# Kernel tuning notes

Hardware: AMD Instinct MI355X
Metric: run time of the kernel (lower is better)

The kernel has to match this reference:

```python
import jax, jax.numpy as jnp
import numpy as np

B, HW, A, N, C = 32, 1600, 5, 128, 80
WIN, HIN = 1280.0, 1280.0
WOUT, HOUT = 40, 40
STRIDE = 32.0
IOU_THRESH = 0.6
OBJECT_SCALE = 5.0
NOOBJECT_SCALE = 1.0
COORD_SCALE = 1.0
CLASS_SCALE = 1.0
ANCHORS = np.array([[1.3221, 1.73145], [3.19275, 4.00944], [5.05587, 8.09892],
                    [9.47112, 4.84053], [11.2364, 10.0071]], dtype=np.float32)


def setup_inputs():
    key = jax.random.key(0)
    k1, k2, k3, k4, k5, k6, k7 = jax.random.split(key, 7)
    bbox_pred = jax.random.uniform(k1, (B, HW, A, 4), jnp.float32)   # sigmoid/exp-decoded preds in [0,1)
    iou_pred = jax.random.uniform(k2, (B, HW, A, 1), jnp.float32)
    x1 = jax.random.uniform(k3, (B, N), jnp.float32) * 1100.0
    y1 = jax.random.uniform(k4, (B, N), jnp.float32) * 1100.0
    wh = jax.random.uniform(k5, (B, N, 2), jnp.float32) * 170.0 + 8.0
    cls = jax.random.randint(k6, (B, N), 0, C).astype(jnp.float32)
    gt_boxes = jnp.stack([x1, y1, x1 + wh[..., 0], y1 + wh[..., 1], cls], axis=-1)  # (B,N,5) in-bounds
    num_boxes = jax.random.randint(k7, (B,), 1, N + 1)
    return {'bbox_pred': bbox_pred, 'iou_pred': iou_pred, 'gt_boxes': gt_boxes,
            'anchors': jnp.asarray(ANCHORS), 'num_boxes': num_boxes, 'size_index': 0}


def _forward(bbox_pred, iou_pred, gt_boxes, anchors, num_boxes, size_index):
    dt = bbox_pred.dtype
    # ---- yolo_to_bbox: decode to absolute (x1,y1,x2,y2) in input pixels ----
    ind = jnp.arange(HW)
    col = (ind % WOUT).astype(dt)[None, :, None]
    row = (ind // WOUT).astype(dt)[None, :, None]
    cxp = (bbox_pred[..., 0] + col) / WOUT
    cyp = (bbox_pred[..., 1] + row) / HOUT
    bw = bbox_pred[..., 2] * anchors[None, None, :, 0] / WOUT * 0.5
    bh = bbox_pred[..., 3] * anchors[None, None, :, 1] / HOUT * 0.5
    scale = jnp.array([WIN, HIN, WIN, HIN], dt)
    real = jnp.stack([cxp - bw, cyp - bh, cxp + bw, cyp + bh], axis=-1) * scale  # (B,HW,A,4)

    # ---- bbox_overlaps_batch: IoU of every decoded box vs every gt ----
    boxes = real.reshape(B, HW * A, 4)
    g = gt_boxes[..., :4]
    barea = (boxes[..., 2] - boxes[..., 0] + 1) * (boxes[..., 3] - boxes[..., 1] + 1)  # (B,K)
    garea = (g[..., 2] - g[..., 0] + 1) * (g[..., 3] - g[..., 1] + 1)                  # (B,N)
    iw = jnp.maximum(jnp.minimum(boxes[:, :, None, 2], g[:, None, :, 2])
                     - jnp.maximum(boxes[:, :, None, 0], g[:, None, :, 0]) + 1, 0.0)
    ih = jnp.maximum(jnp.minimum(boxes[:, :, None, 3], g[:, None, :, 3])
                     - jnp.maximum(boxes[:, :, None, 1], g[:, None, :, 1]) + 1, 0.0)
    inter = iw * ih
    ious = inter / (barea[:, :, None] + garea[:, None, :] - inter)  # (B, HW*A, N)
    ious_r = ious.reshape(B, HW, A, N)
    best = jnp.max(ious, axis=2).reshape(B, HW, A, 1)

    # no-object penalty everywhere best IoU below threshold
    iou_mask = jnp.where(best < IOU_THRESH, NOOBJECT_SCALE * (-iou_pred), jnp.zeros_like(iou_pred))

    # ---- gt -> (cell, anchor) assignment ----
    cx = (gt_boxes[..., 0] + gt_boxes[..., 2]) * 0.5 / STRIDE
    cy = (gt_boxes[..., 1] + gt_boxes[..., 3]) * 0.5 / STRIDE
    cell = (jnp.floor(cy) * WOUT + jnp.floor(cx)).astype(jnp.int32)  # (B,N)
    tw = (gt_boxes[..., 2] - gt_boxes[..., 0] + 1) / STRIDE
    th = (gt_boxes[..., 3] - gt_boxes[..., 1] + 1) / STRIDE
    # anchor_intersections: IoU of co-centered anchors vs stride-normalized gt wh
    gr = g / STRIDE
    gw = gr[..., 2] - gr[..., 0] + 1
    gh = gr[..., 3] - gr[..., 1] + 1
    aw, ah = anchors[:, 0], anchors[:, 1]
    iwa = jnp.minimum(aw[None, :, None], gw[:, None, :])
    iha = jnp.minimum(ah[None, :, None], gh[:, None, :])
    inta = iwa * iha
    a_iou = inta / ((aw * ah)[None, :, None] + (gw * gh)[:, None, :] - inta)  # (B,A,N)
    a_ind = jnp.argmax(a_iou, axis=1)  # (B,N)
    anc = anchors[a_ind]               # (B,N,2)
    tboxes = jnp.stack([cx - jnp.floor(cx), cy - jnp.floor(cy),
                        tw / anc[..., 0], th / anc[..., 1]], axis=-1)  # (B,N,4)

    # ---- vectorized scatter (replaces the python double loop) ----
    valid = (jnp.arange(N)[None, :] < num_boxes[:, None]) & (cell >= 0) & (cell < HW)
    b_idx = jnp.arange(B)[:, None]
    flat = (b_idx * HW + cell) * A + a_ind              # (B,N) index into B*HW*A
    idx = jnp.where(valid, flat, B * HW * A)            # OOB sentinel -> dropped by scatter
    safe = jnp.where(valid, flat, 0)                    # in-bounds index for gathers
    i_idx = jnp.broadcast_to(jnp.arange(N)[None, :], (B, N))

    iou_pred_f = iou_pred.reshape(-1)
    iou_mask = iou_mask.reshape(-1).at[idx].set(
        OBJECT_SCALE * (1.0 - iou_pred_f[safe]), mode='drop').reshape(B, HW, A, 1)
    ious_t = jnp.zeros(B * HW * A, dt).at[idx].set(
        ious_r.reshape(-1)[safe * N + i_idx], mode='drop').reshape(B, HW, A, 1)
    box_mask = jnp.full((B * HW * A,), 0.01, dt).at[idx].set(
        COORD_SCALE, mode='drop').reshape(B, HW, A, 1)
    boxes_t = jnp.broadcast_to(jnp.array([0.5, 0.5, 1.0, 1.0], dt), (B * HW * A, 4)).at[idx].set(
        tboxes, mode='drop').reshape(B, HW, A, 4)
    class_mask = jnp.zeros(B * HW * A, dt).at[idx].set(
        CLASS_SCALE, mode='drop').reshape(B, HW, A, 1)
    cls = gt_boxes[..., 4].astype(jnp.int32)
    idx_c = jnp.where(valid, flat * C + cls, B * HW * A * C)
    classes = jnp.zeros(B * HW * A * C, dt).at[idx_c].set(1.0, mode='drop').reshape(B, HW, A, C)

    return boxes_t, ious_t, classes, box_mask, iou_mask, class_mask


def reference(bbox_pred, iou_pred, gt_boxes, anchors, num_boxes, size_index):
    return _forward(bbox_pred, iou_pred, gt_boxes, anchors, num_boxes, size_index)
```

## Files before the change

### kernel.cpp

```cpp
#include <hip/hip_runtime.h>

#define BB     32
#define HW_    1600
#define AA     5
#define NN     128
#define CC     80
#define WOUT_  40
#define PRED_PER_B (HW_ * AA)

#define OFF_BOXES   0
#define SZ_BOXES    (BB * HW_ * AA * 4)
#define OFF_IOUS    (OFF_BOXES + SZ_BOXES)
#define SZ_IOUS     (BB * HW_ * AA)
#define OFF_CLASSES (OFF_IOUS + SZ_IOUS)
#define SZ_CLASSES  (BB * HW_ * AA * CC)
#define OFF_BMASK   (OFF_CLASSES + SZ_CLASSES)
#define SZ_BMASK    (BB * HW_ * AA)
#define OFF_IMASK   (OFF_BMASK + SZ_BMASK)
#define SZ_IMASK    (BB * HW_ * AA)
#define OFF_CMASK   (OFF_IMASK + SZ_IMASK)
#define SZ_CMASK    (BB * HW_ * AA)

__global__ __launch_bounds__(320) void yolo_passA(
    const float* __restrict__ bbox_pred, const float* __restrict__ iou_pred,
    const float* __restrict__ gt, const float* __restrict__ anchors,
    float* __restrict__ boxes_t, float* __restrict__ ious_t,
    float* __restrict__ classes, float* __restrict__ box_mask,
    float* __restrict__ iou_mask, float* __restrict__ class_mask)
{
    __shared__ float s_g[NN][5];

    const int b     = blockIdx.x / 25;
    const int chunk = blockIdx.x % 25;
    const int tid   = threadIdx.x;

    {
        float4* cbase = reinterpret_cast<float4*>(
            classes + (size_t)(b * PRED_PER_B + chunk * 320) * CC);
        float4 z; z.x = 0.f; z.y = 0.f; z.z = 0.f; z.w = 0.f;
        #pragma unroll
        for (int j = 0; j < 20; ++j)
            cbase[j * 320 + tid] = z;
    }

    for (int n = tid; n < NN; n += 320) {
        const float* gp = gt + (size_t)(b * NN + n) * 5;
        float x1 = gp[0], y1 = gp[1], x2 = gp[2], y2 = gp[3];
        s_g[n][0] = x1; s_g[n][1] = y1; s_g[n][2] = x2; s_g[n][3] = y2;
        float ga = (x2 - x1 + 1.0f) * (y2 - y1 + 1.0f);
        s_g[n][4] = 0.375f * ga;
    }
    __syncthreads();

    const int i  = chunk * 320 + tid;
    const int hw = i / AA;
    const int a  = i - hw * AA;
    const int gid = b * PRED_PER_B + i;

    const float4 p = *reinterpret_cast<const float4*>(bbox_pred + (size_t)gid * 4);
    const float col = (float)(hw % WOUT_);
    const float row = (float)(hw / WOUT_);
    const float aw = anchors[a * 2 + 0];
    const float ah = anchors[a * 2 + 1];

    const float cxp = (p.x + col) / 40.0f;
    const float cyp = (p.y + row) / 40.0f;
    const float bw  = p.z * aw / 40.0f * 0.5f;
    const float bh  = p.w * ah / 40.0f * 0.5f;
    const float px1 = (cxp - bw) * 1280.0f;
    const float py1 = (cyp - bh) * 1280.0f;
    const float px2 = (cxp + bw) * 1280.0f;
    const float py2 = (cyp + bh) * 1280.0f;
    const float barea = (px2 - px1 + 1.0f) * (py2 - py1 + 1.0f);
    const float thrB  = 0.375f * barea;

    bool found = false;
    #pragma unroll 4
    for (int n = 0; n < NN; ++n) {
        float iw = fminf(px2, s_g[n][2]) - fmaxf(px1, s_g[n][0]) + 1.0f;
        iw = fmaxf(iw, 0.0f);
        float ih = fminf(py2, s_g[n][3]) - fmaxf(py1, s_g[n][1]) + 1.0f;
        ih = fmaxf(ih, 0.0f);
        float inter = iw * ih;
        found |= (inter >= thrB + s_g[n][4]);
    }

    iou_mask[gid]   = found ? 0.0f : -iou_pred[gid];
    ious_t[gid]     = 0.0f;
    box_mask[gid]   = 0.01f;
    class_mask[gid] = 0.0f;
    float4 bt; bt.x = 0.5f; bt.y = 0.5f; bt.z = 1.0f; bt.w = 1.0f;
    *reinterpret_cast<float4*>(boxes_t + (size_t)gid * 4) = bt;
}

__global__ __launch_bounds__(128) void yolo_passB(
    const float* __restrict__ bbox_pred, const float* __restrict__ iou_pred,
    const float* __restrict__ gt, const float* __restrict__ anchors,
    const int* __restrict__ num_boxes,
    float* __restrict__ boxes_t, float* __restrict__ ious_t,
    float* __restrict__ classes, float* __restrict__ box_mask,
    float* __restrict__ iou_mask, float* __restrict__ class_mask)
{
    const int b = blockIdx.x;
    const int n = threadIdx.x;

    __shared__ int s_key[NN];

    const float* gp = gt + (size_t)(b * NN + n) * 5;
    const float x1 = gp[0], y1 = gp[1], x2 = gp[2], y2 = gp[3], fc = gp[4];

    const float cx  = (x1 + x2) * 0.5f / 32.0f;
    const float cy  = (y1 + y2) * 0.5f / 32.0f;
    const float fcx = floorf(cx), fcy = floorf(cy);
    const int cell  = (int)(fcy * 40.0f + fcx);
    const float tw  = (x2 - x1 + 1.0f) / 32.0f;
    const float th  = (y2 - y1 + 1.0f) / 32.0f;

    const float gx1 = x1 / 32.0f, gy1 = y1 / 32.0f;
    const float gx2 = x2 / 32.0f, gy2 = y2 / 32.0f;
    const float gw = gx2 - gx1 + 1.0f;
    const float gh = gy2 - gy1 + 1.0f;
    const float gwh = gw * gh;

    int a_ind = 0; float bestA = -1.0f;
    for (int a = 0; a < AA; ++a) {
        float aw = anchors[a * 2 + 0], ah = anchors[a * 2 + 1];
        float iwa = fminf(aw, gw), iha = fminf(ah, gh);
        float inta = iwa * iha;
        float aiou = inta / (aw * ah + gwh - inta);
        if (aiou > bestA) { bestA = aiou; a_ind = a; }
    }
    const float aw = anchors[a_ind * 2 + 0];
    const float ah = anchors[a_ind * 2 + 1];

    const bool valid = (n < num_boxes[b]) && (cell >= 0) && (cell < HW_);
    const int flat = (b * HW_ + cell) * AA + a_ind;

    s_key[n] = valid ? flat : -1;
    __syncthreads();

    if (!valid) return;

    iou_mask[flat]   = 5.0f * (1.0f - iou_pred[flat]);
    box_mask[flat]   = 1.0f;
    class_mask[flat] = 1.0f;
    classes[(size_t)flat * CC + (int)fc] = 1.0f;

    bool winner = true;
    for (int m = n + 1; m < NN; ++m)
        if (s_key[m] == flat) { winner = false; break; }
    if (!winner) return;

    const float* pp = bbox_pred + (size_t)flat * 4;
    const float col = (float)(cell % WOUT_);
    const float rw  = (float)(cell / WOUT_);
    const float cxp = (pp[0] + col) / 40.0f;
    const float cyp = (pp[1] + rw) / 40.0f;
    const float bw  = pp[2] * aw / 40.0f * 0.5f;
    const float bh  = pp[3] * ah / 40.0f * 0.5f;
    const float px1 = (cxp - bw) * 1280.0f;
    const float py1 = (cyp - bh) * 1280.0f;
    const float px2 = (cxp + bw) * 1280.0f;
    const float py2 = (cyp + bh) * 1280.0f;
    const float barea = (px2 - px1 + 1.0f) * (py2 - py1 + 1.0f);
    const float garea = (x2 - x1 + 1.0f) * (y2 - y1 + 1.0f);
    float iw = fmaxf(fminf(px2, x2) - fmaxf(px1, x1) + 1.0f, 0.0f);
    float ih = fmaxf(fminf(py2, y2) - fmaxf(py1, y1) + 1.0f, 0.0f);
    float inter = iw * ih;
    ious_t[flat] = inter / (barea + garea - inter);

    boxes_t[(size_t)flat * 4 + 0] = cx - fcx;
    boxes_t[(size_t)flat * 4 + 1] = cy - fcy;
    boxes_t[(size_t)flat * 4 + 2] = tw / aw;
    boxes_t[(size_t)flat * 4 + 3] = th / ah;
}

extern "C" void kernel_launch(void* const* d_in, const int* in_sizes, int n_in,
                              void* d_out, int out_size, void* d_ws, size_t ws_size,
                              hipStream_t stream) {
    const float* bbox_pred = (const float*)d_in[0];
    const float* iou_pred  = (const float*)d_in[1];
    const float* gt_boxes  = (const float*)d_in[2];
    const float* anchors   = (const float*)d_in[3];
    const int*   num_boxes = (const int*)d_in[4];

    float* out       = (float*)d_out;
    float* boxes_t   = out + OFF_BOXES;
    float* ious_t    = out + OFF_IOUS;
    float* classes   = out + OFF_CLASSES;
    float* box_mask  = out + OFF_BMASK;
    float* iou_mask  = out + OFF_IMASK;
    float* class_mask= out + OFF_CMASK;

    yolo_passA<<<BB * 25, 320, 0, stream>>>(
        bbox_pred, iou_pred, gt_boxes, anchors,
        boxes_t, ious_t, classes, box_mask, iou_mask, class_mask);

    yolo_passB<<<BB, NN, 0, stream>>>(
        bbox_pred, iou_pred, gt_boxes, anchors, num_boxes,
        boxes_t, ious_t, classes, box_mask, iou_mask, class_mask);
}
```

Measured before the change: 136.5 us.

## Fuse gt-assignment pass into prediction pass, removing second kernel launch

Each block now computes anchor matching and target boxes for all ground truths in shared memory. Each prediction thread scans these keys to decide whether it is the assigned cell and writes every output in a single pass. This removes the second launch and its serialization behind the first kernel. In exchange, each block redundantly computes the per-gt assignment and every thread performs an extra 128-entry key scan.

```diff
diff --git a/kernel.cpp b/kernel.cpp
--- a/kernel.cpp
+++ b/kernel.cpp
@@ -15,20 +15,21 @@
 #define OFF_CLASSES (OFF_IOUS + SZ_IOUS)
 #define SZ_CLASSES  (BB * HW_ * AA * CC)
 #define OFF_BMASK   (OFF_CLASSES + SZ_CLASSES)
-#define SZ_BMASK    (BB * HW_ * AA)
-#define OFF_IMASK   (OFF_BMASK + SZ_BMASK)
-#define SZ_IMASK    (BB * HW_ * AA)
-#define OFF_CMASK   (OFF_IMASK + SZ_IMASK)
-#define SZ_CMASK    (BB * HW_ * AA)
+#define OFF_IMASK   (OFF_BMASK + SZ_IOUS)
+#define OFF_CMASK   (OFF_IMASK + SZ_IOUS)
 
-__global__ __launch_bounds__(320) void yolo_passA(
+__global__ __launch_bounds__(320) void yolo_fused(
     const float* __restrict__ bbox_pred, const float* __restrict__ iou_pred,
     const float* __restrict__ gt, const float* __restrict__ anchors,
+    const int* __restrict__ num_boxes,
     float* __restrict__ boxes_t, float* __restrict__ ious_t,
     float* __restrict__ classes, float* __restrict__ box_mask,
     float* __restrict__ iou_mask, float* __restrict__ class_mask)
 {
     __shared__ float s_g[NN][5];
+    __shared__ int   s_key[NN];
+    __shared__ int   s_cls[NN];
+    __shared__ float s_tb[NN][4];
 
     const int b     = blockIdx.x / 25;
     const int chunk = blockIdx.x % 25;
@@ -43,21 +44,52 @@
             cbase[j * 320 + tid] = z;
     }
 
-    for (int n = tid; n < NN; n += 320) {
-        const float* gp = gt + (size_t)(b * NN + n) * 5;
+    if (tid < NN) {
+        const float* gp = gt + (size_t)(b * NN + tid) * 5;
         float x1 = gp[0], y1 = gp[1], x2 = gp[2], y2 = gp[3];
-        s_g[n][0] = x1; s_g[n][1] = y1; s_g[n][2] = x2; s_g[n][3] = y2;
-        float ga = (x2 - x1 + 1.0f) * (y2 - y1 + 1.0f);
-        s_g[n][4] = 0.375f * ga;
+        s_g[tid][0] = x1; s_g[tid][1] = y1; s_g[tid][2] = x2; s_g[tid][3] = y2;
+        s_g[tid][4] = 0.375f * ((x2 - x1 + 1.0f) * (y2 - y1 + 1.0f));
+
+        const float fc = gp[4];
+        const float cx  = (x1 + x2) * 0.5f / 32.0f;
+        const float cy  = (y1 + y2) * 0.5f / 32.0f;
+        const float fcx = floorf(cx), fcy = floorf(cy);
+        const int cell  = (int)(fcy * 40.0f + fcx);
+        const float tw  = (x2 - x1 + 1.0f) / 32.0f;
+        const float th  = (y2 - y1 + 1.0f) / 32.0f;
+
+        const float gw = (x2 / 32.0f) - (x1 / 32.0f) + 1.0f;
+        const float gh = (y2 / 32.0f) - (y1 / 32.0f) + 1.0f;
+        const float gwh = gw * gh;
+
+        int a_ind = 0; float bestA = -1.0f;
+        for (int a = 0; a < AA; ++a) {
+            float aw = anchors[a * 2 + 0], ah = anchors[a * 2 + 1];
+            float iwa = fminf(aw, gw), iha = fminf(ah, gh);
+            float inta = iwa * iha;
+            float aiou = inta / (aw * ah + gwh - inta);
+            if (aiou > bestA) { bestA = aiou; a_ind = a; }
+        }
+        const float aw = anchors[a_ind * 2 + 0];
+        const float ah = anchors[a_ind * 2 + 1];
+
+        const bool valid = (tid < num_boxes[b]) && (cell >= 0) && (cell < HW_);
+        s_key[tid]   = valid ? (cell * AA + a_ind) : -1;
+        s_cls[tid]   = (int)fc;
+        s_tb[tid][0] = cx - fcx;
+        s_tb[tid][1] = cy - fcy;
+        s_tb[tid][2] = tw / aw;
+        s_tb[tid][3] = th / ah;
     }
     __syncthreads();
 
-    const int i  = chunk * 320 + tid;
-    const int hw = i / AA;
-    const int a  = i - hw * AA;
+    const int i   = chunk * 320 + tid;
+    const int hw  = i / AA;
+    const int a   = i - hw * AA;
     const int gid = b * PRED_PER_B + i;
 
-    const float4 p = *reinterpret_cast<const float4*>(bbox_pred + (size_t)gid * 4);
+    const float4 p   = *reinterpret_cast<const float4*>(bbox_pred + (size_t)gid * 4);
+    const float ioup = iou_pred[gid];
     const float col = (float)(hw % WOUT_);
     const float row = (float)(hw / WOUT_);
     const float aw = anchors[a * 2 + 0];
@@ -81,98 +113,39 @@
         iw = fmaxf(iw, 0.0f);
         float ih = fminf(py2, s_g[n][3]) - fmaxf(py1, s_g[n][1]) + 1.0f;
         ih = fmaxf(ih, 0.0f);
-        float inter = iw * ih;
-        found |= (inter >= thrB + s_g[n][4]);
+        found |= (iw * ih >= thrB + s_g[n][4]);
     }
 
-    iou_mask[gid]   = found ? 0.0f : -iou_pred[gid];
-    ious_t[gid]     = 0.0f;
-    box_mask[gid]   = 0.01f;
-    class_mask[gid] = 0.0f;
-    float4 bt; bt.x = 0.5f; bt.y = 0.5f; bt.z = 1.0f; bt.w = 1.0f;
+    int win = -1;
+    for (int m = 0; m < NN; ++m) {
+        if (s_key[m] == i) {
+            classes[(size_t)gid * CC + s_cls[m]] = 1.0f;
+            win = m;
+        }
+    }
+    const bool sc = (win >= 0);
+
+    float iou_w = 0.0f;
+    float4 bt;
+    if (sc) {
+        const float x1 = s_g[win][0], y1 = s_g[win][1];
+        const float x2 = s_g[win][2], y2 = s_g[win][3];
+        const float garea = (x2 - x1 + 1.0f) * (y2 - y1 + 1.0f);
+        float iw = fmaxf(fminf(px2, x2) - fmaxf(px1, x1) + 1.0f, 0.0f);
+        float ih = fmaxf(fminf(py2, y2) - fmaxf(py1, y1) + 1.0f, 0.0f);
+        float inter = iw * ih;
+        iou_w = inter / (barea + garea - inter);
+        bt.x = s_tb[win][0]; bt.y = s_tb[win][1];
+        bt.z = s_tb[win][2]; bt.w = s_tb[win][3];
+    } else {
+        bt.x = 0.5f; bt.y = 0.5f; bt.z = 1.0f; bt.w = 1.0f;
+    }
+
+    iou_mask[gid]   = sc ? 5.0f * (1.0f - ioup) : (found ? 0.0f : -ioup);
+    ious_t[gid]     = iou_w;
+    box_mask[gid]   = sc ? 1.0f : 0.01f;
+    class_mask[gid] = sc ? 1.0f : 0.0f;
     *reinterpret_cast<float4*>(boxes_t + (size_t)gid * 4) = bt;
-}
-
-__global__ __launch_bounds__(128) void yolo_passB(
-    const float* __restrict__ bbox_pred, const float* __restrict__ iou_pred,
-    const float* __restrict__ gt, const float* __restrict__ anchors,
-    const int* __restrict__ num_boxes,
-    float* __restrict__ boxes_t, float* __restrict__ ious_t,
-    float* __restrict__ classes, float* __restrict__ box_mask,
-    float* __restrict__ iou_mask, float* __restrict__ class_mask)
-{
-    const int b = blockIdx.x;
-    const int n = threadIdx.x;
-
-    __shared__ int s_key[NN];
-
-    const float* gp = gt + (size_t)(b * NN + n) * 5;
-    const float x1 = gp[0], y1 = gp[1], x2 = gp[2], y2 = gp[3], fc = gp[4];
-
-    const float cx  = (x1 + x2) * 0.5f / 32.0f;
-    const float cy  = (y1 + y2) * 0.5f / 32.0f;
-    const float fcx = floorf(cx), fcy = floorf(cy);
-    const int cell  = (int)(fcy * 40.0f + fcx);
-    const float tw  = (x2 - x1 + 1.0f) / 32.0f;
-    const float th  = (y2 - y1 + 1.0f) / 32.0f;
-
-    const float gx1 = x1 / 32.0f, gy1 = y1 / 32.0f;
-    const float gx2 = x2 / 32.0f, gy2 = y2 / 32.0f;
-    const float gw = gx2 - gx1 + 1.0f;
-    const float gh = gy2 - gy1 + 1.0f;
-    const float gwh = gw * gh;
-
-    int a_ind = 0; float bestA = -1.0f;
-    for (int a = 0; a < AA; ++a) {
-        float aw = anchors[a * 2 + 0], ah = anchors[a * 2 + 1];
-        float iwa = fminf(aw, gw), iha = fminf(ah, gh);
-        float inta = iwa * iha;
-        float aiou = inta / (aw * ah + gwh - inta);
-        if (aiou > bestA) { bestA = aiou; a_ind = a; }
-    }
-    const float aw = anchors[a_ind * 2 + 0];
-    const float ah = anchors[a_ind * 2 + 1];
-
-    const bool valid = (n < num_boxes[b]) && (cell >= 0) && (cell < HW_);
-    const int flat = (b * HW_ + cell) * AA + a_ind;
-
-    s_key[n] = valid ? flat : -1;
-    __syncthreads();
-
-    if (!valid) return;
-
-    iou_mask[flat]   = 5.0f * (1.0f - iou_pred[flat]);
-    box_mask[flat]   = 1.0f;
-    class_mask[flat] = 1.0f;
-    classes[(size_t)flat * CC + (int)fc] = 1.0f;
-
-    bool winner = true;
-    for (int m = n + 1; m < NN; ++m)
-        if (s_key[m] == flat) { winner = false; break; }
-    if (!winner) return;
-
-    const float* pp = bbox_pred + (size_t)flat * 4;
-    const float col = (float)(cell % WOUT_);
-    const float rw  = (float)(cell / WOUT_);
-    const float cxp = (pp[0] + col) / 40.0f;
-    const float cyp = (pp[1] + rw) / 40.0f;
-    const float bw  = pp[2] * aw / 40.0f * 0.5f;
-    const float bh  = pp[3] * ah / 40.0f * 0.5f;
-    const float px1 = (cxp - bw) * 1280.0f;
-    const float py1 = (cyp - bh) * 1280.0f;
-    const float px2 = (cxp + bw) * 1280.0f;
-    const float py2 = (cyp + bh) * 1280.0f;
-    const float barea = (px2 - px1 + 1.0f) * (py2 - py1 + 1.0f);
-    const float garea = (x2 - x1 + 1.0f) * (y2 - y1 + 1.0f);
-    float iw = fmaxf(fminf(px2, x2) - fmaxf(px1, x1) + 1.0f, 0.0f);
-    float ih = fmaxf(fminf(py2, y2) - fmaxf(py1, y1) + 1.0f, 0.0f);
-    float inter = iw * ih;
-    ious_t[flat] = inter / (barea + garea - inter);
-
-    boxes_t[(size_t)flat * 4 + 0] = cx - fcx;
-    boxes_t[(size_t)flat * 4 + 1] = cy - fcy;
-    boxes_t[(size_t)flat * 4 + 2] = tw / aw;
-    boxes_t[(size_t)flat * 4 + 3] = th / ah;
 }
 
 extern "C" void kernel_launch(void* const* d_in, const int* in_sizes, int n_in,
@@ -184,19 +157,9 @@
     const float* anchors   = (const float*)d_in[3];
     const int*   num_boxes = (const int*)d_in[4];
 
-    float* out       = (float*)d_out;
-    float* boxes_t   = out + OFF_BOXES;
-    float* ious_t    = out + OFF_IOUS;
-    float* classes   = out + OFF_CLASSES;
-    float* box_mask  = out + OFF_BMASK;
-    float* iou_mask  = out + OFF_IMASK;
-    float* class_mask= out + OFF_CMASK;
-
-    yolo_passA<<<BB * 25, 320, 0, stream>>>(
-        bbox_pred, iou_pred, gt_boxes, anchors,
-        boxes_t, ious_t, classes, box_mask, iou_mask, class_mask);
-
-    yolo_passB<<<BB, NN, 0, stream>>>(
+    float* out = (float*)d_out;
+    yolo_fused<<<BB * 25, 320, 0, stream>>>(
         bbox_pred, iou_pred, gt_boxes, anchors, num_boxes,
-        boxes_t, ious_t, classes, box_mask, iou_mask, class_mask);
+        out + OFF_BOXES, out + OFF_IOUS, out + OFF_CLASSES,
+        out + OFF_BMASK, out + OFF_IMASK, out + OFF_CMASK);
 }
```

After: 128.8 us. 1.06x faster.
